# Kernel tuning notes

Measured on AMD Instinct MI355X. Metric: run time of the kernel, lower is better.

The kernel has to match this reference:

```python
import jax, jax.numpy as jnp
import numpy as np

B, NQ, NK, D, H = 2, 1024, 1024, 512, 32


def setup_inputs() -> dict:
    key = jax.random.key(0)
    ks = jax.random.split(key, 6)
    keys_t = jax.random.normal(ks[0], (B, NK, D), dtype=jnp.float32)
    queries = jax.random.normal(ks[1], (B, NQ, D), dtype=jnp.float32)
    # torch nn.Linear default init: U(-1/sqrt(fan_in), 1/sqrt(fan_in))
    s1 = 1.0 / np.sqrt(2 * D)
    W1 = jax.random.uniform(ks[2], (2 * D, H), jnp.float32, -s1, s1)  # (2d, hidden)
    b1 = jax.random.uniform(ks[3], (H,), jnp.float32, -s1, s1)
    s2 = 1.0 / np.sqrt(H)
    W2 = jax.random.uniform(ks[4], (H, 1), jnp.float32, -s2, s2)
    b2 = jax.random.uniform(ks[5], (1,), jnp.float32, -s2, s2)
    return {"keys": keys_t, "queries": queries, "W1": W1, "b1": b1, "W2": W2, "b2": b2}


def reference(keys, queries, W1, b1, W2, b2):
    # logits[b,q,k] = W2 . tanh(W1 @ cat(keys[b,k], queries[b,q]) + b1) + b2
    # Decompose first linear: cat(k,q) @ W1 == k @ W1[:D] + q @ W1[D:]
    d = keys.shape[-1]
    hk = jnp.einsum('bkd,dh->bkh', keys, W1[:d])      # (B, NK, H)
    hq = jnp.einsum('bqd,dh->bqh', queries, W1[d:])   # (B, NQ, H)
    h = jnp.tanh(hk[:, None, :, :] + hq[:, :, None, :] + b1)  # (B, NQ, NK, H)
    logits = jnp.einsum('bqkh,ho->bqko', h, W2)[..., 0] + b2[0]  # (B, NQ, NK)
    return logits
```

## Files before the change

### kernel.cpp

```cpp
#include <hip/hip_runtime.h>

#define NB 2
#define NQS 1024
#define NKS 1024
#define DD 512
#define HH 32
#define NROW (NB * NKS)

static __device__ __forceinline__ float fexp2(float x) {
#if __has_builtin(__builtin_amdgcn_exp2f)
  return __builtin_amdgcn_exp2f(x);
#else
  float r; asm("v_exp_f32 %0, %1" : "=v"(r) : "v"(x)); return r;
#endif
}
static __device__ __forceinline__ float frcp(float x) {
#if __has_builtin(__builtin_amdgcn_rcpf)
  return __builtin_amdgcn_rcpf(x);
#else
  float r; asm("v_rcp_f32 %0, %1" : "=v"(r) : "v"(x)); return r;
#endif
}

__global__ __launch_bounds__(256) void p1_proj(
    const float* __restrict__ keys, const float* __restrict__ queries,
    const float* __restrict__ W1, const float* __restrict__ b1,
    float* __restrict__ E) {
  const float S = 2.8853900817779268f;
  const int tid = threadIdx.x;
  const int hg = tid & 7;
  const int dq = (tid >> 3) & 3;
  const int row = blockIdx.x * 8 + (tid >> 5);
  const bool isq = row >= NROW;
  const float* src = (isq ? queries + (size_t)(row - NROW) * DD
                          : keys + (size_t)row * DD) + dq * 128;
  const float* w1 = W1 + ((size_t)(isq ? DD : 0) + dq * 128) * HH + hg * 4;
  float4 a0 = {0.f, 0.f, 0.f, 0.f}, a1 = {0.f, 0.f, 0.f, 0.f};
#pragma unroll 4
  for (int i = 0; i < 32; ++i) {
    float4 s4 = *(const float4*)(src + i * 4);
    const float* wp = w1 + (size_t)i * 4 * HH;
    float4 w0 = *(const float4*)(wp);
    float4 wv1 = *(const float4*)(wp + HH);
    float4 wv2 = *(const float4*)(wp + 2 * HH);
    float4 wv3 = *(const float4*)(wp + 3 * HH);
    a0.x = fmaf(s4.x, w0.x, a0.x);  a0.y = fmaf(s4.x, w0.y, a0.y);
    a0.z = fmaf(s4.x, w0.z, a0.z);  a0.w = fmaf(s4.x, w0.w, a0.w);
    a1.x = fmaf(s4.y, wv1.x, a1.x); a1.y = fmaf(s4.y, wv1.y, a1.y);
    a1.z = fmaf(s4.y, wv1.z, a1.z); a1.w = fmaf(s4.y, wv1.w, a1.w);
    a0.x = fmaf(s4.z, wv2.x, a0.x); a0.y = fmaf(s4.z, wv2.y, a0.y);
    a0.z = fmaf(s4.z, wv2.z, a0.z); a0.w = fmaf(s4.z, wv2.w, a0.w);
    a1.x = fmaf(s4.w, wv3.x, a1.x); a1.y = fmaf(s4.w, wv3.y, a1.y);
    a1.z = fmaf(s4.w, wv3.z, a1.z); a1.w = fmaf(s4.w, wv3.w, a1.w);
  }
  a0.x += a1.x; a0.y += a1.y; a0.z += a1.z; a0.w += a1.w;
  a0.x += __shfl_xor(a0.x, 8);  a0.y += __shfl_xor(a0.y, 8);
  a0.z += __shfl_xor(a0.z, 8);  a0.w += __shfl_xor(a0.w, 8);
  a0.x += __shfl_xor(a0.x, 16); a0.y += __shfl_xor(a0.y, 16);
  a0.z += __shfl_xor(a0.z, 16); a0.w += __shfl_xor(a0.w, 16);
  if ((tid & 24) == 0) {
    float bx = 0.f, by = 0.f, bz = 0.f, bw = 0.f;
    if (isq) {
      const float4 bb = *(const float4*)(b1 + hg * 4);
      bx = bb.x; by = bb.y; bz = bb.z; bw = bb.w;
    }
    float4 o;
    o.x = fexp2(S * (a0.x + bx));
    o.y = fexp2(S * (a0.y + by));
    o.z = fexp2(S * (a0.z + bz));
    o.w = fexp2(S * (a0.w + bw));
    *(float4*)(E + (size_t)row * HH + hg * 4) = o;
  }
}

__global__ __launch_bounds__(256) void p2_score(
    const float* __restrict__ E, const float* __restrict__ W2,
    const float* __restrict__ b2, float* __restrict__ out) {
  __shared__ float EkL[64 * 33];
  __shared__ float EqL[64 * 32];
  const int tid = threadIdx.x;
  const int k0 = blockIdx.x * 64, q0 = blockIdx.y * 64, b = blockIdx.z;
  const float* Ek_g = E + (size_t)(b * NKS + k0) * HH;
  const float* Eq_g = E + (size_t)NROW * HH + (size_t)(b * NQS + q0) * HH;
#pragma unroll
  for (int j = 0; j < 2; ++j) {
    int i = j * 1024 + tid * 4;
    *(float4*)(EqL + i) = *(const float4*)(Eq_g + i);
    float4 w = *(const float4*)(Ek_g + i);
    int r = i >> 5, c = i & 31;
    EkL[r * 33 + c + 0] = w.x;
    EkL[r * 33 + c + 1] = w.y;
    EkL[r * 33 + c + 2] = w.z;
    EkL[r * 33 + c + 3] = w.w;
  }
  float w2n[HH];
  float c0 = b2[0];
#pragma unroll
  for (int h = 0; h < HH; ++h) {
    float w = W2[h];
    c0 += w;
    w2n[h] = -2.f * w;
  }
  __syncthreads();
  const int kl = tid & 63, qg = tid >> 6;
  float ek[HH];
#pragma unroll
  for (int h = 0; h < HH; ++h) ek[h] = EkL[kl * 33 + h];
  float* outp = out + (size_t)(b * NQS + q0 + qg * 16) * NKS + k0 + kl;
  const float* eqrow = EqL + qg * 16 * HH;
  for (int j = 0; j < 16; ++j) {
    float acc0 = c0, acc1 = 0.f;
    const float4* e4 = (const float4*)(eqrow + (size_t)j * HH);
#pragma unroll
    for (int h0 = 0; h0 < 8; ++h0) {
      float4 ev = e4[h0];
      acc0 = fmaf(w2n[h0 * 4 + 0], frcp(fmaf(ek[h0 * 4 + 0], ev.x, 1.f)), acc0);
      acc1 = fmaf(w2n[h0 * 4 + 1], frcp(fmaf(ek[h0 * 4 + 1], ev.y, 1.f)), acc1);
      acc0 = fmaf(w2n[h0 * 4 + 2], frcp(fmaf(ek[h0 * 4 + 2], ev.z, 1.f)), acc0);
      acc1 = fmaf(w2n[h0 * 4 + 3], frcp(fmaf(ek[h0 * 4 + 3], ev.w, 1.f)), acc1);
    }
    outp[(size_t)j * NKS] = acc0 + acc1;
  }
}

extern "C" void kernel_launch(void* const* d_in, const int* in_sizes, int n_in,
                              void* d_out, int out_size, void* d_ws, size_t ws_size,
                              hipStream_t stream) {
  const float* keys = (const float*)d_in[0];
  const float* queries = (const float*)d_in[1];
  const float* W1 = (const float*)d_in[2];
  const float* b1 = (const float*)d_in[3];
  const float* W2 = (const float*)d_in[4];
  const float* b2 = (const float*)d_in[5];
  float* out = (float*)d_out;
  float* ws = (float*)d_ws;

  hipLaunchKernelGGL(p1_proj, dim3(512), dim3(256), 0, stream,
                     keys, queries, W1, b1, ws);
  hipLaunchKernelGGL(p2_score, dim3(NKS / 64, NQS / 64, NB), dim3(256), 0, stream,
                     ws, W2, b2, out);
}
```

Before: 25.84 us.

## Pair tanh terms to halve reciprocals and move projection to bf16 MFMA

The score kernel merges pairs of hidden units into a single fraction over a shared denominator. This halves the number of reciprocal instructions, which are transcendental, at the cost of a few extra FMAs. The q-tile shrinks from 64 to 32 rows, doubling the number of blocks. The projection kernel now uses bf16 16x16x32 MFMA instructions with 64-thread blocks, which lowers precision on the inputs and the W1 weights. Multiplying two denominators could overflow when the exponentials are large.

```diff
diff --git a/kernel.cpp b/kernel.cpp
--- a/kernel.cpp
+++ b/kernel.cpp
@@ -1,11 +1,15 @@
 #include <hip/hip_runtime.h>
+#include <hip/hip_bf16.h>
 
 #define NB 2
 #define NQS 1024
 #define NKS 1024
 #define DD 512
 #define HH 32
-#define NROW (NB * NKS)
+#define NKROW (NB * NKS)
+
+typedef __attribute__((ext_vector_type(8))) short bf16x8;
+typedef __attribute__((ext_vector_type(4))) float f32x4;
 
 static __device__ __forceinline__ float fexp2(float x) {
 #if __has_builtin(__builtin_amdgcn_exp2f)
@@ -22,54 +26,46 @@
 #endif
 }
 
-__global__ __launch_bounds__(256) void p1_proj(
+__global__ __launch_bounds__(64) void p1_proj_mfma(
     const float* __restrict__ keys, const float* __restrict__ queries,
     const float* __restrict__ W1, const float* __restrict__ b1,
     float* __restrict__ E) {
   const float S = 2.8853900817779268f;
-  const int tid = threadIdx.x;
-  const int hg = tid & 7;
-  const int dq = (tid >> 3) & 3;
-  const int row = blockIdx.x * 8 + (tid >> 5);
-  const bool isq = row >= NROW;
-  const float* src = (isq ? queries + (size_t)(row - NROW) * DD
-                          : keys + (size_t)row * DD) + dq * 128;
-  const float* w1 = W1 + ((size_t)(isq ? DD : 0) + dq * 128) * HH + hg * 4;
-  float4 a0 = {0.f, 0.f, 0.f, 0.f}, a1 = {0.f, 0.f, 0.f, 0.f};
-#pragma unroll 4
-  for (int i = 0; i < 32; ++i) {
-    float4 s4 = *(const float4*)(src + i * 4);
-    const float* wp = w1 + (size_t)i * 4 * HH;
-    float4 w0 = *(const float4*)(wp);
-    float4 wv1 = *(const float4*)(wp + HH);
-    float4 wv2 = *(const float4*)(wp + 2 * HH);
-    float4 wv3 = *(const float4*)(wp + 3 * HH);
-    a0.x = fmaf(s4.x, w0.x, a0.x);  a0.y = fmaf(s4.x, w0.y, a0.y);
-    a0.z = fmaf(s4.x, w0.z, a0.z);  a0.w = fmaf(s4.x, w0.w, a0.w);
-    a1.x = fmaf(s4.y, wv1.x, a1.x); a1.y = fmaf(s4.y, wv1.y, a1.y);
-    a1.z = fmaf(s4.y, wv1.z, a1.z); a1.w = fmaf(s4.y, wv1.w, a1.w);
-    a0.x = fmaf(s4.z, wv2.x, a0.x); a0.y = fmaf(s4.z, wv2.y, a0.y);
-    a0.z = fmaf(s4.z, wv2.z, a0.z); a0.w = fmaf(s4.z, wv2.w, a0.w);
-    a1.x = fmaf(s4.w, wv3.x, a1.x); a1.y = fmaf(s4.w, wv3.y, a1.y);
-    a1.z = fmaf(s4.w, wv3.z, a1.z); a1.w = fmaf(s4.w, wv3.w, a1.w);
+  const int l = threadIdx.x;
+  const int row0 = blockIdx.x * 16;
+  const bool isq = row0 >= NKROW;
+  const float* src = isq ? (queries + (size_t)(row0 - NKROW) * DD)
+                         : (keys + (size_t)row0 * DD);
+  const float* w1 = W1 + (isq ? (size_t)DD * HH : (size_t)0);
+  const int m = l & 15, kq = l >> 4;
+  f32x4 acc0 = {0.f, 0.f, 0.f, 0.f}, acc1 = {0.f, 0.f, 0.f, 0.f};
+  const float* arow = src + (size_t)m * DD + kq * 8;
+#pragma unroll 2
+  for (int s = 0; s < 16; ++s) {
+    const int kb = s * 32 + kq * 8;
+    float4 a0 = *(const float4*)(arow + s * 32);
+    float4 a1 = *(const float4*)(arow + s * 32 + 4);
+    union { bf16x8 v; __hip_bfloat16 e[8]; } af, bf0, bf1;
+    af.e[0] = __float2bfloat16(a0.x); af.e[1] = __float2bfloat16(a0.y);
+    af.e[2] = __float2bfloat16(a0.z); af.e[3] = __float2bfloat16(a0.w);
+    af.e[4] = __float2bfloat16(a1.x); af.e[5] = __float2bfloat16(a1.y);
+    af.e[6] = __float2bfloat16(a1.z); af.e[7] = __float2bfloat16(a1.w);
+    const float* wk = w1 + (size_t)kb * HH;
+#pragma unroll
+    for (int j = 0; j < 8; ++j) {
+      bf0.e[j] = __float2bfloat16(wk[j * HH + m]);
+      bf1.e[j] = __float2bfloat16(wk[j * HH + 16 + m]);
+    }
+    acc0 = __builtin_amdgcn_mfma_f32_16x16x32_bf16(af.v, bf0.v, acc0, 0, 0, 0);
+    acc1 = __builtin_amdgcn_mfma_f32_16x16x32_bf16(af.v, bf1.v, acc1, 0, 0, 0);
   }
-  a0.x += a1.x; a0.y += a1.y; a0.z += a1.z; a0.w += a1.w;
-  a0.x += __shfl_xor(a0.x, 8);  a0.y += __shfl_xor(a0.y, 8);
-  a0.z += __shfl_xor(a0.z, 8);  a0.w += __shfl_xor(a0.w, 8);
-  a0.x += __shfl_xor(a0.x, 16); a0.y += __shfl_xor(a0.y, 16);
-  a0.z += __shfl_xor(a0.z, 16); a0.w += __shfl_xor(a0.w, 16);
-  if ((tid & 24) == 0) {
-    float bx = 0.f, by = 0.f, bz = 0.f, bw = 0.f;
-    if (isq) {
-      const float4 bb = *(const float4*)(b1 + hg * 4);
-      bx = bb.x; by = bb.y; bz = bb.z; bw = bb.w;
-    }
-    float4 o;
-    o.x = fexp2(S * (a0.x + bx));
-    o.y = fexp2(S * (a0.y + by));
-    o.z = fexp2(S * (a0.z + bz));
-    o.w = fexp2(S * (a0.w + bw));
-    *(float4*)(E + (size_t)row * HH + hg * 4) = o;
+  float bias0 = 0.f, bias1 = 0.f;
+  if (isq) { bias0 = b1[m]; bias1 = b1[16 + m]; }
+#pragma unroll
+  for (int r = 0; r < 4; ++r) {
+    const int rr = row0 + kq * 4 + r;
+    E[(size_t)rr * HH + m]      = fexp2(S * (acc0[r] + bias0));
+    E[(size_t)rr * HH + 16 + m] = fexp2(S * (acc1[r] + bias1));
   }
 }
 
@@ -77,47 +73,65 @@
     const float* __restrict__ E, const float* __restrict__ W2,
     const float* __restrict__ b2, float* __restrict__ out) {
   __shared__ float EkL[64 * 33];
-  __shared__ float EqL[64 * 32];
+  __shared__ float EqL[32 * 32];
   const int tid = threadIdx.x;
-  const int k0 = blockIdx.x * 64, q0 = blockIdx.y * 64, b = blockIdx.z;
+  const int k0 = blockIdx.x * 64, q0 = blockIdx.y * 32, b = blockIdx.z;
   const float* Ek_g = E + (size_t)(b * NKS + k0) * HH;
-  const float* Eq_g = E + (size_t)NROW * HH + (size_t)(b * NQS + q0) * HH;
-#pragma unroll
-  for (int j = 0; j < 2; ++j) {
-    int i = j * 1024 + tid * 4;
-    *(float4*)(EqL + i) = *(const float4*)(Eq_g + i);
+  const float* Eq_g = E + (size_t)NKROW * HH + (size_t)(b * NQS + q0) * HH;
+  {
+    int i = tid * 4;
     float4 w = *(const float4*)(Ek_g + i);
     int r = i >> 5, c = i & 31;
-    EkL[r * 33 + c + 0] = w.x;
-    EkL[r * 33 + c + 1] = w.y;
-    EkL[r * 33 + c + 2] = w.z;
-    EkL[r * 33 + c + 3] = w.w;
+    EkL[r * 33 + c + 0] = w.x; EkL[r * 33 + c + 1] = w.y;
+    EkL[r * 33 + c + 2] = w.z; EkL[r * 33 + c + 3] = w.w;
+    i += 1024;
+    w = *(const float4*)(Ek_g + i);
+    r = i >> 5; c = i & 31;
+    EkL[r * 33 + c + 0] = w.x; EkL[r * 33 + c + 1] = w.y;
+    EkL[r * 33 + c + 2] = w.z; EkL[r * 33 + c + 3] = w.w;
+    *(float4*)(EqL + tid * 4) = *(const float4*)(Eq_g + tid * 4);
   }
-  float w2n[HH];
   float c0 = b2[0];
+  float w2v[HH];
 #pragma unroll
-  for (int h = 0; h < HH; ++h) {
-    float w = W2[h];
-    c0 += w;
-    w2n[h] = -2.f * w;
-  }
+  for (int h = 0; h < HH; ++h) { float w = W2[h]; c0 += w; w2v[h] = -2.f * w; }
+  float C01[16];
+#pragma unroll
+  for (int i = 0; i < 16; ++i) C01[i] = w2v[2 * i] + w2v[2 * i + 1];
   __syncthreads();
   const int kl = tid & 63, qg = tid >> 6;
   float ek[HH];
 #pragma unroll
   for (int h = 0; h < HH; ++h) ek[h] = EkL[kl * 33 + h];
-  float* outp = out + (size_t)(b * NQS + q0 + qg * 16) * NKS + k0 + kl;
-  const float* eqrow = EqL + qg * 16 * HH;
-  for (int j = 0; j < 16; ++j) {
+  float Aa[16], Bb[16];
+#pragma unroll
+  for (int i = 0; i < 16; ++i) {
+    Aa[i] = w2v[2 * i] * ek[2 * i + 1];
+    Bb[i] = w2v[2 * i + 1] * ek[2 * i];
+  }
+  float* outp = out + (size_t)(b * NQS + q0 + qg * 8) * NKS + k0 + kl;
+  const float* eqrow = EqL + qg * 8 * HH;
+#pragma unroll 2
+  for (int j = 0; j < 8; ++j) {
     float acc0 = c0, acc1 = 0.f;
     const float4* e4 = (const float4*)(eqrow + (size_t)j * HH);
 #pragma unroll
-    for (int h0 = 0; h0 < 8; ++h0) {
-      float4 ev = e4[h0];
-      acc0 = fmaf(w2n[h0 * 4 + 0], frcp(fmaf(ek[h0 * 4 + 0], ev.x, 1.f)), acc0);
-      acc1 = fmaf(w2n[h0 * 4 + 1], frcp(fmaf(ek[h0 * 4 + 1], ev.y, 1.f)), acc1);
-      acc0 = fmaf(w2n[h0 * 4 + 2], frcp(fmaf(ek[h0 * 4 + 2], ev.z, 1.f)), acc0);
-      acc1 = fmaf(w2n[h0 * 4 + 3], frcp(fmaf(ek[h0 * 4 + 3], ev.w, 1.f)), acc1);
+    for (int i2 = 0; i2 < 8; ++i2) {
+      float4 ev = e4[i2];
+      {
+        const int i = 2 * i2;
+        float da = fmaf(ek[2 * i], ev.x, 1.f);
+        float db = fmaf(ek[2 * i + 1], ev.y, 1.f);
+        float num = fmaf(Aa[i], ev.y, fmaf(Bb[i], ev.x, C01[i]));
+        acc0 = fmaf(num, frcp(da * db), acc0);
+      }
+      {
+        const int i = 2 * i2 + 1;
+        float da = fmaf(ek[2 * i], ev.z, 1.f);
+        float db = fmaf(ek[2 * i + 1], ev.w, 1.f);
+        float num = fmaf(Aa[i], ev.w, fmaf(Bb[i], ev.z, C01[i]));
+        acc1 = fmaf(num, frcp(da * db), acc1);
+      }
     }
     outp[(size_t)j * NKS] = acc0 + acc1;
   }
@@ -135,8 +149,8 @@
   float* out = (float*)d_out;
   float* ws = (float*)d_ws;
 
-  hipLaunchKernelGGL(p1_proj, dim3(512), dim3(256), 0, stream,
+  hipLaunchKernelGGL(p1_proj_mfma, dim3(256), dim3(64), 0, stream,
                      keys, queries, W1, b1, ws);
-  hipLaunchKernelGGL(p2_score, dim3(NKS / 64, NQS / 64, NB), dim3(256), 0, stream,
+  hipLaunchKernelGGL(p2_score, dim3(NKS / 64, NQS / 32, NB), dim3(256), 0, stream,
                      ws, W2, b2, out);
 }
```

New measurement: 22.92 us. 1.13x faster.
